# Optimization experiments

Hardware: AMD Instinct MI355X
Metric: run time of the kernel (lower is better)

The kernel has to match this reference:

```python
import jax, jax.numpy as jnp
import numpy as np

DIM = 1024
N_HEADS = 16
N_KV = 4
HEAD_DIM = 64
HIDDEN = 2048
N_EXP = 8
TOP_K = 2
B, T = 2, 1024
EPS = 1e-6


def rmsnorm(x, w):
    rms = jnp.sqrt(jnp.mean(x * x, axis=-1, keepdims=True) + EPS)
    return w * x / rms


def apply_rope(x, cos, sin):
    # x: [B, H, T, D]; cos/sin: [T, D//2]
    Tn = x.shape[2]
    c = cos[None, None, :Tn, :]
    s = sin[None, None, :Tn, :]
    xe = x[..., 0::2]
    xo = x[..., 1::2]
    re = xe * c - xo * s
    ro = xe * s + xo * c
    return jnp.stack([re, ro], axis=-1).reshape(x.shape)


def setup_inputs() -> dict:
    key = jax.random.key(0)
    ks = jax.random.split(key, 12)
    sd = DIM ** -0.5
    x = jax.random.normal(ks[0], (B, T, DIM), dtype=jnp.float32)
    # RoPE tables
    half = HEAD_DIM // 2
    inv_freq = 1.0 / (10000.0 ** (np.arange(0, half, dtype=np.float32) / half))
    pos = np.arange(T, dtype=np.float32)
    ang = np.outer(pos, inv_freq)
    cos = jnp.asarray(np.cos(ang), dtype=jnp.float32)
    sin = jnp.asarray(np.sin(ang), dtype=jnp.float32)
    return {
        "x": x,
        "cos": cos,
        "sin": sin,
        "norm_attn_w": jnp.ones((DIM,), jnp.float32),
        "wq": jax.random.normal(ks[1], (N_HEADS * HEAD_DIM, DIM), jnp.float32) * sd,
        "wk": jax.random.normal(ks[2], (N_KV * HEAD_DIM, DIM), jnp.float32) * sd,
        "wv": jax.random.normal(ks[3], (N_KV * HEAD_DIM, DIM), jnp.float32) * sd,
        "wo": jax.random.normal(ks[4], (DIM, N_HEADS * HEAD_DIM), jnp.float32) * sd,
        "norm_ffn_w": jnp.ones((DIM,), jnp.float32),
        "router_w": jax.random.normal(ks[5], (N_EXP, DIM), jnp.float32) * sd,
        "router_b": jnp.zeros((N_EXP,), jnp.float32),
        "w_gate": jax.random.normal(ks[6], (N_EXP, HIDDEN, DIM), jnp.float32) * sd,
        "w_up": jax.random.normal(ks[7], (N_EXP, HIDDEN, DIM), jnp.float32) * sd,
        "w_down": jax.random.normal(ks[8], (N_EXP, DIM, HIDDEN), jnp.float32) * (HIDDEN ** -0.5),
    }


def attention(x, cos, sin, wq, wk, wv, wo):
    Bn, Tn, _ = x.shape
    q = (x @ wq.T).reshape(Bn, Tn, N_HEADS, HEAD_DIM).transpose(0, 2, 1, 3)
    k = (x @ wk.T).reshape(Bn, Tn, N_KV, HEAD_DIM).transpose(0, 2, 1, 3)
    v = (x @ wv.T).reshape(Bn, Tn, N_KV, HEAD_DIM).transpose(0, 2, 1, 3)
    q = apply_rope(q, cos, sin)
    k = apply_rope(k, cos, sin)
    rep = N_HEADS // N_KV
    k = jnp.repeat(k, rep, axis=1)
    v = jnp.repeat(v, rep, axis=1)
    scale = HEAD_DIM ** -0.5
    scores = jnp.einsum("bhqd,bhkd->bhqk", q, k) * scale
    causal = jnp.triu(jnp.ones((Tn, Tn), dtype=bool), k=1)
    scores = jnp.where(causal[None, None], -jnp.inf, scores)
    attn = jax.nn.softmax(scores, axis=-1)
    out = jnp.einsum("bhqk,bhkd->bhqd", attn, v)
    out = out.transpose(0, 2, 1, 3).reshape(Bn, Tn, N_HEADS * HEAD_DIM)
    return out @ wo.T


def moe(x, router_w, router_b, w_gate, w_up, w_down):
    Bn, Tn, D = x.shape
    flat = x.reshape(-1, D)  # [N, D]
    N = flat.shape[0]
    logits = flat @ router_w.T + router_b
    probs = jax.nn.softmax(logits, axis=-1)
    top_vals, top_idx = jax.lax.top_k(probs, TOP_K)
    top_vals = top_vals / (jnp.sum(top_vals, axis=-1, keepdims=True) + 1e-9)
    # combine weights [N, E]
    comb = jnp.zeros((N, N_EXP), flat.dtype).at[jnp.arange(N)[:, None], top_idx].add(top_vals)
    g = jnp.einsum("nd,ehd->enh", flat, w_gate)
    u = jnp.einsum("nd,ehd->enh", flat, w_up)
    h = jax.nn.silu(g) * u
    eo = jnp.einsum("enh,edh->end", h, w_down)  # [E, N, D]
    out = jnp.einsum("ne,end->nd", comb, eo)
    return out.reshape(Bn, Tn, D)


def reference(x, cos, sin, norm_attn_w, wq, wk, wv, wo, norm_ffn_w, router_w, router_b, w_gate, w_up, w_down):
    x = x + attention(rmsnorm(x, norm_attn_w), cos, sin, wq, wk, wv, wo)
    x = x + moe(rmsnorm(x, norm_ffn_w), router_w, router_b, w_gate, w_up, w_down)
    return x
```

## Files before the change

kernel.cpp:

```cpp
#include <hip/hip_runtime.h>
#include <math.h>

#define N_TOK   2048
#define SEQ     1024
#define DIMM    1024
#define NH      16
#define NKV     4
#define HD      64
#define HID     2048
#define NEXP    8
#define QKVW    1536

typedef __attribute__((ext_vector_type(4))) float f32x4;
typedef __attribute__((ext_vector_type(8))) short s16x8;
typedef unsigned short u16;

__device__ __forceinline__ u16 f2bf(float f) {
    union { float f; unsigned u; } v; v.f = f;
    unsigned r = v.u + 0x7fffu + ((v.u >> 16) & 1u);
    return (u16)(r >> 16);
}
__device__ __forceinline__ float bf2f(u16 h) {
    union { unsigned u; float f; } v; v.u = ((unsigned)h) << 16;
    return v.f;
}

__device__ __forceinline__ f32x4 mfma16(s16x8 a, s16x8 b, f32x4 c) {
    return __builtin_amdgcn_mfma_f32_16x16x32_bf16(a, b, c, 0, 0, 0);
}

__device__ __forceinline__ int lds_byte(int row, int byte_in_row, int swz_key) {
    return row * 128 + (byte_in_row ^ ((swz_key & 7) << 4));
}

__device__ __forceinline__ s16x8 ldfrag(const char* base, int row, int ks, int lane) {
    int b = lds_byte(row, ks * 64 + ((lane >> 4) * 16), row);
    return *(const s16x8*)(base + b);
}

__device__ __forceinline__ void gload16(const void* g, void* l) {
    __builtin_amdgcn_global_load_lds(
        (const __attribute__((address_space(1))) void*)g,
        (__attribute__((address_space(3))) void*)l, 16, 0, 0);
}

__global__ __launch_bounds__(256) void prep1(const float* __restrict__ wq,
    const float* __restrict__ wk, const float* __restrict__ wv, const float* __restrict__ wo,
    u16* __restrict__ hi, u16* __restrict__ lo,
    const float* __restrict__ x, const float* __restrict__ w_na,
    u16* __restrict__ oh, u16* __restrict__ ol)
{
    if (blockIdx.x < 1024) {
        int i = blockIdx.x * 256 + threadIdx.x;
        int stride = 1024 * 256;
        for (; i < 655360; i += stride) {
            const float* in; int j;
            if (i < 262144)      { in = wq; j = i; }
            else if (i < 327680) { in = wk; j = i - 262144; }
            else if (i < 393216) { in = wv; j = i - 327680; }
            else                 { in = wo; j = i - 393216; }
            f32x4 v = __builtin_nontemporal_load((const f32x4*)in + j);
            ushort4 h, l;
            h.x = f2bf(v[0]); h.y = f2bf(v[1]); h.z = f2bf(v[2]); h.w = f2bf(v[3]);
            l.x = f2bf(v[0] - bf2f(h.x)); l.y = f2bf(v[1] - bf2f(h.y));
            l.z = f2bf(v[2] - bf2f(h.z)); l.w = f2bf(v[3] - bf2f(h.w));
            reinterpret_cast<ushort4*>(hi)[i] = h;
            reinterpret_cast<ushort4*>(lo)[i] = l;
        }
    } else {
        int row = blockIdx.x - 1024;
        const float4* xr = reinterpret_cast<const float4*>(x + (size_t)row * DIMM);
        const float4* wr = reinterpret_cast<const float4*>(w_na);
        float4 v = xr[threadIdx.x];
        float ss = v.x*v.x + v.y*v.y + v.z*v.z + v.w*v.w;
#pragma unroll
        for (int off = 32; off; off >>= 1) ss += __shfl_xor(ss, off);
        __shared__ float red[4];
        int wid = threadIdx.x >> 6, lane = threadIdx.x & 63;
        if (lane == 0) red[wid] = ss;
        __syncthreads();
        float tot = red[0] + red[1] + red[2] + red[3];
        float inv = rsqrtf(tot * (1.0f/DIMM) + 1e-6f);
        float4 ww = wr[threadIdx.x];
        float4 o;
        o.x = ww.x * v.x * inv;
        o.y = ww.y * v.y * inv;
        o.z = ww.z * v.z * inv;
        o.w = ww.w * v.w * inv;
        ushort4 h, l;
        h.x = f2bf(o.x); h.y = f2bf(o.y); h.z = f2bf(o.z); h.w = f2bf(o.w);
        l.x = f2bf(o.x - bf2f(h.x)); l.y = f2bf(o.y - bf2f(h.y));
        l.z = f2bf(o.z - bf2f(h.z)); l.w = f2bf(o.w - bf2f(h.w));
        reinterpret_cast<ushort4*>(oh + (size_t)row * DIMM)[threadIdx.x] = h;
        reinterpret_cast<ushort4*>(ol + (size_t)row * DIMM)[threadIdx.x] = l;
    }
}

__global__ __launch_bounds__(256) void rmsnorm_router(const float* __restrict__ x,
    const float* __restrict__ w, const float* __restrict__ rw, const float* __restrict__ rb,
    u16* __restrict__ outb, int* __restrict__ top_idx, float* __restrict__ top_w)
{
    int row = blockIdx.x;
    int tid = threadIdx.x;
    int wid = tid >> 6, lane = tid & 63;
    const float4* xr = reinterpret_cast<const float4*>(x + (size_t)row * DIMM);
    const float4* wr = reinterpret_cast<const float4*>(w);
    float4 v = xr[tid];
    float ss = v.x*v.x + v.y*v.y + v.z*v.z + v.w*v.w;
#pragma unroll
    for (int off = 32; off; off >>= 1) ss += __shfl_xor(ss, off);
    __shared__ float red[4];
    __shared__ float lred[4][NEXP];
    if (lane == 0) red[wid] = ss;
    __syncthreads();
    float tot = red[0] + red[1] + red[2] + red[3];
    float inv = rsqrtf(tot * (1.0f/DIMM) + 1e-6f);
    float4 ww = wr[tid];
    float4 o;
    o.x = ww.x * v.x * inv;
    o.y = ww.y * v.y * inv;
    o.z = ww.z * v.z * inv;
    o.w = ww.w * v.w * inv;
    ushort4 ob;
    ob.x = f2bf(o.x); ob.y = f2bf(o.y); ob.z = f2bf(o.z); ob.w = f2bf(o.w);
    reinterpret_cast<ushort4*>(outb + (size_t)row * DIMM)[tid] = ob;
    float acc[NEXP];
#pragma unroll
    for (int e = 0; e < NEXP; e++) {
        float4 r4 = reinterpret_cast<const float4*>(rw + (size_t)e * DIMM)[tid];
        acc[e] = o.x * r4.x + o.y * r4.y + o.z * r4.z + o.w * r4.w;
    }
#pragma unroll
    for (int e = 0; e < NEXP; e++) {
        float p = acc[e];
#pragma unroll
        for (int off = 32; off; off >>= 1) p += __shfl_xor(p, off);
        acc[e] = p;
    }
    if (lane == 0)
#pragma unroll
        for (int e = 0; e < NEXP; e++) lred[wid][e] = acc[e];
    __syncthreads();
    if (tid == 0) {
        float lg[NEXP];
#pragma unroll
        for (int e = 0; e < NEXP; e++)
            lg[e] = lred[0][e] + lred[1][e] + lred[2][e] + lred[3][e] + rb[e];
        float m = lg[0];
#pragma unroll
        for (int e = 1; e < NEXP; e++) m = fmaxf(m, lg[e]);
        float pe[NEXP], s = 0.f;
#pragma unroll
        for (int e = 0; e < NEXP; e++) { pe[e] = __expf(lg[e] - m); s += pe[e]; }
        int i1 = 0; float v1 = pe[0];
#pragma unroll
        for (int e = 1; e < NEXP; e++) if (pe[e] > v1) { v1 = pe[e]; i1 = e; }
        int i2 = -1; float v2 = -1.f;
#pragma unroll
        for (int e = 0; e < NEXP; e++) if (e != i1 && pe[e] > v2) { v2 = pe[e]; i2 = e; }
        v1 /= s; v2 /= s;
        float den = v1 + v2 + 1e-9f;
        top_idx[2 * row] = i1; top_idx[2 * row + 1] = i2;
        top_w[2 * row] = v1 / den; top_w[2 * row + 1] = v2 / den;
    }
}

__global__ __launch_bounds__(256) void route_build(const int* __restrict__ top_idx,
    const float* __restrict__ top_w, int* __restrict__ counts, int* __restrict__ offs,
    int* __restrict__ assign_token, float* __restrict__ assign_w)
{
    __shared__ int lcnt[NEXP], loff[NEXP], lpos[NEXP];
    int tid = threadIdx.x;
    if (tid < NEXP) { lcnt[tid] = 0; lpos[tid] = 0; }
    __syncthreads();
    for (int i = tid; i < 2 * N_TOK; i += 256)
        atomicAdd(&lcnt[top_idx[i]], 1);
    __syncthreads();
    if (tid == 0) {
        int s = 0;
        for (int e = 0; e < NEXP; e++) { loff[e] = s; s += lcnt[e]; }
    }
    __syncthreads();
    if (tid < NEXP) { counts[tid] = lcnt[tid]; offs[tid] = loff[tid]; }
    for (int i = tid; i < 2 * N_TOK; i += 256) {
        int e = top_idx[i];
        int p = atomicAdd(&lpos[e], 1);
        int r = loff[e] + p;
        assign_token[r] = i >> 1;
        assign_w[r] = top_w[i];
    }
}

__global__ __launch_bounds__(256) void gemm_bs(const u16* __restrict__ Ah_,
    const u16* __restrict__ Al_, const u16* __restrict__ Bh_, const u16* __restrict__ Bl_,
    float* __restrict__ C, const float* __restrict__ R, int M, int N, int K, int ldc)
{
    __shared__ __align__(16) u16 Ah[128 * 64], Al[128 * 64];
    __shared__ __align__(16) u16 Bh[64 * 64],  Bl[64 * 64];
    int tid = threadIdx.x;
    int m0 = blockIdx.y * 128, n0 = blockIdx.x * 64;
    int lane = tid & 63, wv = tid >> 6;
    int wm = wv >> 1, wn = wv & 1;
    int sr = lane >> 3, sc = lane & 7;

    f32x4 acc[4][2];
#pragma unroll
    for (int i = 0; i < 4; i++)
#pragma unroll
        for (int j = 0; j < 2; j++) acc[i][j] = f32x4{0.f, 0.f, 0.f, 0.f};

    const int NT = K >> 6;
    int bid = blockIdx.x + gridDim.x * blockIdx.y;
    int ph = (bid * 5) & (NT - 1);

    for (int tt = 0; tt < NT; ++tt) {
        int k0 = ((tt + ph) & (NT - 1)) << 6;
#pragma unroll
        for (int i = 0; i < 4; i++) {
            int row = wv * 32 + i * 8 + sr;
            int c = sc ^ (row & 7);
            size_t g = (size_t)(m0 + row) * K + k0 + c * 8;
            gload16(Ah_ + g, (void*)(Ah + (wv * 4 + i) * 512));
            gload16(Al_ + g, (void*)(Al + (wv * 4 + i) * 512));
        }
#pragma unroll
        for (int i = 0; i < 2; i++) {
            int row = wv * 16 + i * 8 + sr;
            int c = sc ^ (row & 7);
            size_t g = (size_t)(n0 + row) * K + k0 + c * 8;
            gload16(Bh_ + g, (void*)(Bh + (wv * 2 + i) * 512));
            gload16(Bl_ + g, (void*)(Bl + (wv * 2 + i) * 512));
        }
        __syncthreads();
#pragma unroll
        for (int ks = 0; ks < 2; ++ks) {
            s16x8 afh[4], afl[4], bfh[2], bfl[2];
#pragma unroll
            for (int mi = 0; mi < 4; mi++) {
                int row = wm * 64 + mi * 16 + (lane & 15);
                afh[mi] = ldfrag((const char*)Ah, row, ks, lane);
                afl[mi] = ldfrag((const char*)Al, row, ks, lane);
            }
#pragma unroll
            for (int nj = 0; nj < 2; nj++) {
                int row = wn * 32 + nj * 16 + (lane & 15);
                bfh[nj] = ldfrag((const char*)Bh, row, ks, lane);
                bfl[nj] = ldfrag((const char*)Bl, row, ks, lane);
            }
#pragma unroll
            for (int mi = 0; mi < 4; mi++)
#pragma unroll
                for (int nj = 0; nj < 2; nj++) {
                    acc[mi][nj] = mfma16(afl[mi], bfh[nj], acc[mi][nj]);
                    acc[mi][nj] = mfma16(afh[mi], bfl[nj], acc[mi][nj]);
                    acc[mi][nj] = mfma16(afh[mi], bfh[nj], acc[mi][nj]);
                }
        }
        __syncthreads();
    }
#pragma unroll
    for (int mi = 0; mi < 4; mi++)
#pragma unroll
        for (int nj = 0; nj < 2; nj++)
#pragma unroll
            for (int r = 0; r < 4; r++) {
                int m = m0 + wm * 64 + mi * 16 + (lane >> 4) * 4 + r;
                int n = n0 + wn * 32 + nj * 16 + (lane & 15);
                float v = acc[mi][nj][r];
                if (R) v += R[(size_t)m * ldc + n];
                C[(size_t)m * ldc + n] = v;
            }
}

__global__ __launch_bounds__(256) void prep2(const float* __restrict__ qkvb,
    const float* __restrict__ cs, const float* __restrict__ sn,
    u16* __restrict__ qsh, u16* __restrict__ qsl,
    u16* __restrict__ ksh, u16* __restrict__ ksl,
    u16* __restrict__ vth, u16* __restrict__ vtl)
{
    const int ROPE_BLOCKS = (N_TOK * (NH + NKV) * 32) / 256;
    if (blockIdx.x < ROPE_BLOCKS) {
        int gid = blockIdx.x * 256 + threadIdx.x;
        const int QTOT = N_TOK * NH * 32;
        int nheads, base_col, out_w;
        u16 *oh, *ol;
        if (gid < QTOT) {
            nheads = NH; base_col = 0; out_w = NH * HD; oh = qsh; ol = qsl;
        } else {
            gid -= QTOT;
            nheads = NKV; base_col = 1024; out_w = NKV * HD; oh = ksh; ol = ksl;
        }
        int i = gid & 31;
        int h = (gid >> 5) % nheads;
        int n = gid / (32 * nheads);
        int t = n & (SEQ - 1);
        const float* p = qkvb + (size_t)n * QKVW + base_col + h * HD + 2 * i;
        float xe = p[0], xo = p[1];
        float c = cs[t * 32 + i], s = sn[t * 32 + i];
        float re = xe * c - xo * s;
        float ro = xe * s + xo * c;
        size_t o = (size_t)n * out_w + h * HD + 2 * i;
        u16 reh = f2bf(re), roh = f2bf(ro);
        oh[o] = reh;     oh[o + 1] = roh;
        ol[o] = f2bf(re - bf2f(reh));
        ol[o + 1] = f2bf(ro - bf2f(roh));
    } else {
        __shared__ float t[64][65];
        int r = blockIdx.x - ROPE_BLOCKS;
        int bx = r & 31;
        int by = r >> 5;
        int tid = threadIdx.x;
        int c4 = tid & 15, r0 = tid >> 4;
#pragma unroll
        for (int i = 0; i < 4; i++) {
            int row = r0 + i * 16;
            float4 vv = *(const float4*)(qkvb + (size_t)(bx * 64 + row) * QKVW + 1280 + by * 64 + c4 * 4);
            t[c4 * 4 + 0][row] = vv.x;
            t[c4 * 4 + 1][row] = vv.y;
            t[c4 * 4 + 2][row] = vv.z;
            t[c4 * 4 + 3][row] = vv.w;
        }
        __syncthreads();
#pragma unroll
        for (int i = 0; i < 4; i++) {
            int drow = r0 + i * 16;
            ushort4 hh, ll;
            float a = t[drow][c4 * 4 + 0], b = t[drow][c4 * 4 + 1];
            float c = t[drow][c4 * 4 + 2], d = t[drow][c4 * 4 + 3];
            hh.x = f2bf(a); hh.y = f2bf(b); hh.z = f2bf(c); hh.w = f2bf(d);
            ll.x = f2bf(a - bf2f(hh.x)); ll.y = f2bf(b - bf2f(hh.y));
            ll.z = f2bf(c - bf2f(hh.z)); ll.w = f2bf(d - bf2f(hh.w));
            size_t o = ((size_t)(by * 64 + drow) * N_TOK + bx * 64 + c4 * 4) >> 2;
            reinterpret_cast<ushort4*>(vth)[o] = hh;
            reinterpret_cast<ushort4*>(vtl)[o] = ll;
        }
    }
}

__global__ __launch_bounds__(256) void attn_cvt(const u16* __restrict__ qsh,
    const u16* __restrict__ qsl, const u16* __restrict__ ksh, const u16* __restrict__ ksl,
    const u16* __restrict__ vth, const u16* __restrict__ vtl,
    u16* __restrict__ outh, u16* __restrict__ outl,
    const float* __restrict__ wg, const float* __restrict__ wu, const float* __restrict__ wd,
    u16* __restrict__ wgb, u16* __restrict__ wub, u16* __restrict__ wdb)
{
    if (blockIdx.x >= 512) {
        const int n4 = 4 << 20;
        int i = (blockIdx.x - 512) * 1024 + threadIdx.x;
        int stride = 3072 * 1024;
        for (; i < 3 * n4; i += stride) {
            int seg = i >> 22;
            int j = i & (n4 - 1);
            const f32x4* in = (const f32x4*)((seg == 0) ? wg : (seg == 1) ? wu : wd);
            ushort4* out = (ushort4*)((seg == 0) ? wgb : (seg == 1) ? wub : wdb);
            f32x4 v0 = __builtin_nontemporal_load(in + j);
            f32x4 v1 = __builtin_nontemporal_load(in + j + 256);
            f32x4 v2 = __builtin_nontemporal_load(in + j + 512);
            f32x4 v3 = __builtin_nontemporal_load(in + j + 768);
            ushort4 o0, o1, o2, o3;
            o0.x = f2bf(v0[0]); o0.y = f2bf(v0[1]); o0.z = f2bf(v0[2]); o0.w = f2bf(v0[3]);
            o1.x = f2bf(v1[0]); o1.y = f2bf(v1[1]); o1.z = f2bf(v1[2]); o1.w = f2bf(v1[3]);
            o2.x = f2bf(v2[0]); o2.y = f2bf(v2[1]); o2.z = f2bf(v2[2]); o2.w = f2bf(v2[3]);
            o3.x = f2bf(v3[0]); o3.y = f2bf(v3[1]); o3.z = f2bf(v3[2]); o3.w = f2bf(v3[3]);
            out[j]       = o0;
            out[j + 256] = o1;
            out[j + 512] = o2;
            out[j + 768] = o3;
        }
        return;
    }
    int bi = blockIdx.x;
    int b = bi >> 8;
    int h = (bi >> 4) & 15;
    int qt = 15 - (bi & 15);
    int kvh = h >> 2;
    int tid = threadIdx.x;
    int lane = tid & 63, wv = tid >> 6;
    int q0 = qt * 64;
    int sr = lane >> 3, sc = lane & 7;

    __shared__ __align__(16) u16 Qh[64 * 64], Ql[64 * 64];
    __shared__ __align__(16) u16 Kh[64 * 64], Kl[64 * 64];
    __shared__ __align__(16) u16 Vh[64 * 64], Vl[64 * 64];

#pragma unroll
    for (int i = 0; i < 2; i++) {
        int row = wv * 16 + i * 8 + sr;
        int c = sc ^ (row & 7);
        size_t g = (size_t)(b * SEQ + q0 + row) * (NH * HD) + h * HD + c * 8;
        gload16(qsh + g, (void*)(Qh + (wv * 2 + i) * 512));
        gload16(qsl + g, (void*)(Ql + (wv * 2 + i) * 512));
    }
    __syncthreads();

    s16x8 aQh[2], aQl[2];
#pragma unroll
    for (int ks = 0; ks < 2; ks++) {
        aQh[ks] = ldfrag((const char*)Qh, wv * 16 + (lane & 15), ks, lane);
        aQl[ks] = ldfrag((const char*)Ql, wv * 16 + (lane & 15), ks, lane);
    }

    float m_run[4], l_run[4];
    f32x4 acc_o[4];
#pragma unroll
    for (int r = 0; r < 4; r++) { m_run[r] = -1e30f; l_run[r] = 0.f; }
#pragma unroll
    for (int nj = 0; nj < 4; nj++) acc_o[nj] = f32x4{0.f, 0.f, 0.f, 0.f};

    for (int kt = 0; kt <= qt; kt++) {
        int kbase = kt * 64;
        __syncthreads();
#pragma unroll
        for (int i = 0; i < 2; i++) {
            int row = wv * 16 + i * 8 + sr;
            int c = sc ^ (row & 7);
            size_t gk = (size_t)(b * SEQ + kbase + row) * (NKV * HD) + kvh * HD + c * 8;
            size_t gv = (size_t)(kvh * HD + row) * N_TOK + b * SEQ + kbase + c * 8;
            gload16(ksh + gk, (void*)(Kh + (wv * 2 + i) * 512));
            gload16(ksl + gk, (void*)(Kl + (wv * 2 + i) * 512));
            gload16(vth + gv, (void*)(Vh + (wv * 2 + i) * 512));
            gload16(vtl + gv, (void*)(Vl + (wv * 2 + i) * 512));
        }
        __syncthreads();

        f32x4 sacc[4];
#pragma unroll
        for (int nj = 0; nj < 4; nj++) sacc[nj] = f32x4{0.f, 0.f, 0.f, 0.f};
#pragma unroll
        for (int ks = 0; ks < 2; ks++) {
#pragma unroll
            for (int nj = 0; nj < 4; nj++) {
                s16x8 bKh = ldfrag((const char*)Kh, nj * 16 + (lane & 15), ks, lane);
                s16x8 bKl = ldfrag((const char*)Kl, nj * 16 + (lane & 15), ks, lane);
                sacc[nj] = mfma16(aQl[ks], bKh, sacc[nj]);
                sacc[nj] = mfma16(aQh[ks], bKl, sacc[nj]);
                sacc[nj] = mfma16(aQh[ks], bKh, sacc[nj]);
            }
        }

        float sv[4][4];
#pragma unroll
        for (int nj = 0; nj < 4; nj++)
#pragma unroll
            for (int r = 0; r < 4; r++) {
                float s = sacc[nj][r] * 0.125f;
                if (kt == qt) {
                    int row_loc = wv * 16 + (lane >> 4) * 4 + r;
                    int col_loc = nj * 16 + (lane & 15);
                    if (col_loc > row_loc) s = -1e30f;
                }
                sv[nj][r] = s;
            }

        float p[4][4];
#pragma unroll
        for (int r = 0; r < 4; r++) {
            float mx = fmaxf(fmaxf(sv[0][r], sv[1][r]), fmaxf(sv[2][r], sv[3][r]));
            mx = fmaxf(mx, __shfl_xor(mx, 1));
            mx = fmaxf(mx, __shfl_xor(mx, 2));
            mx = fmaxf(mx, __shfl_xor(mx, 4));
            mx = fmaxf(mx, __shfl_xor(mx, 8));
            float m_new = fmaxf(m_run[r], mx);
            float corr = __expf(m_run[r] - m_new);
            float ps = 0.f;
#pragma unroll
            for (int nj = 0; nj < 4; nj++) {
                float pv = __expf(sv[nj][r] - m_new);
                p[nj][r] = pv;
                ps += pv;
            }
            ps += __shfl_xor(ps, 1);
            ps += __shfl_xor(ps, 2);
            ps += __shfl_xor(ps, 4);
            ps += __shfl_xor(ps, 8);
            l_run[r] = l_run[r] * corr + ps;
            m_run[r] = m_new;
#pragma unroll
            for (int nj = 0; nj < 4; nj++) acc_o[nj][r] *= corr;
        }

        char* phb = (char*)Qh + wv * 2048;
        char* plb = (char*)Ql + wv * 2048;
#pragma unroll
        for (int nj = 0; nj < 4; nj++)
#pragma unroll
            for (int r = 0; r < 4; r++) {
                int row = (lane >> 4) * 4 + r;
                int col = nj * 16 + (lane & 15);
                u16 hh = f2bf(p[nj][r]);
                u16 ll = f2bf(p[nj][r] - bf2f(hh));
                int byte = lds_byte(row, col * 2, row);
                *(u16*)(phb + byte) = hh;
                *(u16*)(plb + byte) = ll;
            }

#pragma unroll
        for (int ks = 0; ks < 2; ks++) {
            s16x8 aPh = ldfrag(phb, lane & 15, ks, lane);
            s16x8 aPl = ldfrag(plb, lane & 15, ks, lane);
#pragma unroll
            for (int nj = 0; nj < 4; nj++) {
                s16x8 bVh = ldfrag((const char*)Vh, nj * 16 + (lane & 15), ks, lane);
                s16x8 bVl = ldfrag((const char*)Vl, nj * 16 + (lane & 15), ks, lane);
                acc_o[nj] = mfma16(aPl, bVh, acc_o[nj]);
                acc_o[nj] = mfma16(aPh, bVl, acc_o[nj]);
                acc_o[nj] = mfma16(aPh, bVh, acc_o[nj]);
            }
        }
    }

#pragma unroll
    for (int r = 0; r < 4; r++) {
        int row_glob = q0 + wv * 16 + (lane >> 4) * 4 + r;
        float inv = 1.f / l_run[r];
#pragma unroll
        for (int nj = 0; nj < 4; nj++) {
            int dv = nj * 16 + (lane & 15);
            size_t idx = (size_t)(b * SEQ + row_glob) * (NH * HD) + h * HD + dv;
            float v = acc_o[nj][r] * inv;
            u16 hh = f2bf(v);
            outh[idx] = hh;
            outl[idx] = f2bf(v - bf2f(hh));
        }
    }
}

__global__ __launch_bounds__(256) void moe_gateup2(const u16* __restrict__ xb,
    const u16* __restrict__ wgb, const u16* __restrict__ wub,
    const int* __restrict__ assign_token, const int* __restrict__ offs,
    const int* __restrict__ counts, u16* __restrict__ hbufb)
{
    int e = blockIdx.z;
    int cnt = counts[e];
    int t0 = blockIdx.y * 128;
    if (t0 >= cnt) return;
    int base = offs[e];
    int h0 = blockIdx.x * 64;
    __shared__ __align__(16) u16 As[128 * 64];
    __shared__ __align__(16) u16 Gs[64 * 64];
    __shared__ __align__(16) u16 Us[64 * 64];
    __shared__ int toks[128];
    int tid = threadIdx.x;
    if (tid < 128) {
        int a = t0 + tid;
        toks[tid] = (a < cnt) ? assign_token[base + a] : 0;
    }
    __syncthreads();
    int lane = tid & 63, wv = tid >> 6;
    int wm = wv >> 1, wn = wv & 1;
    int sr = lane >> 3, sc = lane & 7;

    int tokr[4];
#pragma unroll
    for (int i = 0; i < 4; i++) tokr[i] = toks[wv * 32 + i * 8 + sr];

    const u16* wge = wgb + (size_t)e * HID * DIMM;
    const u16* wue = wub + (size_t)e * HID * DIMM;

    f32x4 accg[4][2], accu[4][2];
#pragma unroll
    for (int i = 0; i < 4; i++)
#pragma unroll
        for (int j = 0; j < 2; j++) { accg[i][j] = f32x4{0,0,0,0}; accu[i][j] = f32x4{0,0,0,0}; }

    const int NT = DIMM / 64;
    int bid = blockIdx.x + gridDim.x * (blockIdx.y + gridDim.y * blockIdx.z);
    int ph = (bid * 5) & (NT - 1);

    for (int tt = 0; tt < NT; ++tt) {
        int k0 = ((tt + ph) & (NT - 1)) << 6;
#pragma unroll
        for (int i = 0; i < 4; i++) {
            int row = wv * 32 + i * 8 + sr;
            int c = sc ^ (row & 7);
            gload16(xb + (size_t)tokr[i] * DIMM + k0 + c * 8, (void*)(As + (wv * 4 + i) * 512));
        }
#pragma unroll
        for (int i = 0; i < 2; i++) {
            int row = wv * 16 + i * 8 + sr;
            int c = sc ^ (row & 7);
            gload16(wge + (size_t)(h0 + row) * DIMM + k0 + c * 8, (void*)(Gs + (wv * 2 + i) * 512));
            gload16(wue + (size_t)(h0 + row) * DIMM + k0 + c * 8, (void*)(Us + (wv * 2 + i) * 512));
        }
        __syncthreads();
#pragma unroll
        for (int ks = 0; ks < 2; ++ks) {
            s16x8 af[4], gf[2], uf[2];
#pragma unroll
            for (int mi = 0; mi < 4; mi++)
                af[mi] = ldfrag((const char*)As, wm * 64 + mi * 16 + (lane & 15), ks, lane);
#pragma unroll
            for (int nj = 0; nj < 2; nj++) {
                int row = wn * 32 + nj * 16 + (lane & 15);
                gf[nj] = ldfrag((const char*)Gs, row, ks, lane);
                uf[nj] = ldfrag((const char*)Us, row, ks, lane);
            }
#pragma unroll
            for (int mi = 0; mi < 4; mi++)
#pragma unroll
                for (int nj = 0; nj < 2; nj++) {
                    accg[mi][nj] = mfma16(af[mi], gf[nj], accg[mi][nj]);
                    accu[mi][nj] = mfma16(af[mi], uf[nj], accu[mi][nj]);
                }
        }
        __syncthreads();
    }
#pragma unroll
    for (int mi = 0; mi < 4; mi++)
#pragma unroll
        for (int nj = 0; nj < 2; nj++)
#pragma unroll
            for (int r = 0; r < 4; r++) {
                int row = wm * 64 + mi * 16 + (lane >> 4) * 4 + r;
                if (t0 + row < cnt) {
                    int col = wn * 32 + nj * 16 + (lane & 15);
                    float g = accg[mi][nj][r], u = accu[mi][nj][r];
                    float hh = (g / (1.f + __expf(-g))) * u;
                    hbufb[(size_t)(base + t0 + row) * HID + h0 + col] = f2bf(hh);
                }
            }
}

__global__ __launch_bounds__(256) void moe_down2(const u16* __restrict__ hbufb,
    const u16* __restrict__ wdb, const int* __restrict__ assign_token,
    const float* __restrict__ assign_w, const int* __restrict__ offs,
    const int* __restrict__ counts, float* __restrict__ out)
{
    int e = blockIdx.z;
    int cnt = counts[e];
    int t0 = blockIdx.y * 128;
    if (t0 >= cnt) return;
    int base = offs[e];
    int d0 = blockIdx.x * 128;
    __shared__ __align__(16) u16 As[128 * 64];
    __shared__ __align__(16) u16 Bs[128 * 64];
    __shared__ int toks[128];
    __shared__ float rw_[128];
    int tid = threadIdx.x;
    if (tid < 128) {
        int a = t0 + tid;
        toks[tid] = (a < cnt) ? assign_token[base + a] : 0;
        rw_[tid] = (a < cnt) ? assign_w[base + a] : 0.f;
    }
    __syncthreads();
    int lane = tid & 63, wv = tid >> 6;
    int wm = wv >> 1, wn = wv & 1;
    int sr = lane >> 3, sc = lane & 7;

    const u16* wde = wdb + (size_t)e * DIMM * HID;

    f32x4 acc[4][4];
#pragma unroll
    for (int i = 0; i < 4; i++)
#pragma unroll
        for (int j = 0; j < 4; j++) acc[i][j] = f32x4{0,0,0,0};

    const int NT = HID / 64;
    int bid = blockIdx.x + gridDim.x * (blockIdx.y + gridDim.y * blockIdx.z);
    int ph = (bid * 5) & (NT - 1);

    for (int tt = 0; tt < NT; ++tt) {
        int k0 = ((tt + ph) & (NT - 1)) << 6;
#pragma unroll
        for (int i = 0; i < 4; i++) {
            int row = wv * 32 + i * 8 + sr;
            int c = sc ^ (row & 7);
            gload16(hbufb + (size_t)(base + t0 + row) * HID + k0 + c * 8, (void*)(As + (wv * 4 + i) * 512));
            gload16(wde + (size_t)(d0 + row) * HID + k0 + c * 8, (void*)(Bs + (wv * 4 + i) * 512));
        }
        __syncthreads();
#pragma unroll
        for (int ks = 0; ks < 2; ++ks) {
            s16x8 af[4];
#pragma unroll
            for (int mi = 0; mi < 4; mi++)
                af[mi] = ldfrag((const char*)As, wm * 64 + mi * 16 + (lane & 15), ks, lane);
#pragma unroll
            for (int nj = 0; nj < 4; nj++) {
                s16x8 bf = ldfrag((const char*)Bs, wn * 64 + nj * 16 + (lane & 15), ks, lane);
#pragma unroll
                for (int mi = 0; mi < 4; mi++)
                    acc[mi][nj] = mfma16(af[mi], bf, acc[mi][nj]);
            }
        }
        __syncthreads();
    }
#pragma unroll
    for (int mi = 0; mi < 4; mi++)
#pragma unroll
        for (int r = 0; r < 4; r++) {
            int row = wm * 64 + mi * 16 + (lane >> 4) * 4 + r;
            if (t0 + row < cnt) {
                int tok = toks[row];
                float w = rw_[row];
#pragma unroll
                for (int nj = 0; nj < 4; nj++) {
                    int col = d0 + wn * 64 + nj * 16 + (lane & 15);
                    atomicAdd(&out[(size_t)tok * DIMM + col], acc[mi][nj][r] * w);
                }
            }
        }
}

extern "C" void kernel_launch(void* const* d_in, const int* in_sizes, int n_in,
                              void* d_out, int out_size, void* d_ws, size_t ws_size,
                              hipStream_t stream)
{
    const float* x      = (const float*)d_in[0];
    const float* cs     = (const float*)d_in[1];
    const float* sn     = (const float*)d_in[2];
    const float* w_na   = (const float*)d_in[3];
    const float* wq     = (const float*)d_in[4];
    const float* wk     = (const float*)d_in[5];
    const float* wv     = (const float*)d_in[6];
    const float* wo     = (const float*)d_in[7];
    const float* w_nf   = (const float*)d_in[8];
    const float* rw     = (const float*)d_in[9];
    const float* rb     = (const float*)d_in[10];
    const float* wg     = (const float*)d_in[11];
    const float* wu     = (const float*)d_in[12];
    const float* wd     = (const float*)d_in[13];
    float* out = (float*)d_out;

    const size_t F = 1024 * 1024;
    float* wsf = (float*)d_ws;

    float* qkvb = wsf;
    float* tail = wsf + 3 * F;
    u16* qsh    = (u16*)(wsf + 3 * F + F / 2);
    u16* qsl    = (u16*)(wsf + 4 * F + F / 2);
    u16* ksh    = (u16*)(wsf + 5 * F + F / 2);
    u16* ksl    = (u16*)(wsf + 5 * F + 3 * F / 4);
    u16* vth    = (u16*)(wsf + 6 * F);
    u16* vtl    = (u16*)(wsf + 6 * F + F / 4);
    u16* xn2b   = (u16*)(wsf + 6 * F + F / 2);
    u16* hbufb  = (u16*)(wsf + 7 * F + F / 2);
    u16* xnh    = (u16*)(wsf + 7 * F + F / 2);
    u16* xnl    = (u16*)(wsf + 8 * F + F / 2);
    u16* attnh  = (u16*)(wsf + 9 * F + F / 2);
    u16* attnl  = (u16*)(wsf + 10 * F + F / 2);
    u16* wgb    = (u16*)(wsf + 11 * F + F / 2);
    u16* wub    = (u16*)(wsf + 19 * F + F / 2);
    u16* wdb    = (u16*)(wsf + 27 * F + F / 2);
    u16* wqkvoh = (u16*)(wsf + 35 * F + F / 2);
    u16* wqkvol = (u16*)(wsf + 36 * F + 3 * F / 4);

    int*   top_idx      = (int*)tail;
    float* top_w        = tail + 4096;
    int*   counts       = (int*)(tail + 8192);
    int*   offs         = (int*)(tail + 8192) + 8;
    int*   assign_token = (int*)(tail + 8192) + 32;
    float* assign_w     = tail + 8192 + 32 + 4096;

    prep1<<<3072, 256, 0, stream>>>(wq, wk, wv, wo, wqkvoh, wqkvol, x, w_na, xnh, xnl);
    gemm_bs<<<dim3(QKVW / 64, 16), 256, 0, stream>>>(xnh, xnl, wqkvoh, wqkvol,
                                                     qkvb, nullptr, N_TOK, QKVW, DIMM, QKVW);
    prep2<<<5248, 256, 0, stream>>>(qkvb, cs, sn, qsh, qsl, ksh, ksl, vth, vtl);
    attn_cvt<<<3584, 256, 0, stream>>>(qsh, qsl, ksh, ksl, vth, vtl, attnh, attnl,
                                       wg, wu, wd, wgb, wub, wdb);
    gemm_bs<<<dim3(DIMM / 64, 16), 256, 0, stream>>>(attnh, attnl,
                                                     wqkvoh + (size_t)1536 * 1024, wqkvol + (size_t)1536 * 1024,
                                                     out, x, N_TOK, DIMM, NH * HD, DIMM);
    rmsnorm_router<<<N_TOK, 256, 0, stream>>>(out, w_nf, rw, rb, xn2b, top_idx, top_w);
    route_build<<<1, 256, 0, stream>>>(top_idx, top_w, counts, offs, assign_token, assign_w);
    moe_gateup2<<<dim3(HID / 64, 16, NEXP), 256, 0, stream>>>(xn2b, wgb, wub, assign_token, offs, counts, hbufb);
    moe_down2<<<dim3(DIMM / 128, 16, NEXP), 256, 0, stream>>>(hbufb, wdb, assign_token, assign_w, offs, counts, out);
}
```

Baseline: 314.5 us.

## Spread MoE weight bf16 conversion across QKV gemm, attention and out-proj kernels

The fp32-to-bf16 conversion of the expert weights used to run only as extra blocks inside the attention kernel. It is now split into three ranges, handled by extra blocks appended to the QKV projection GEMM, the attention kernel and the output projection GEMM. The GEMM grid is flattened to 1D so conversion blocks can share the launch. The aim is to hide the memory-bound conversion behind the compute-bound kernels. The risk is that conversion traffic slows the GEMMs, and the extra blocks change how blocks are scheduled.

Result: faster. 302.2 us, median of 2 (-3.9%).

```diff
diff --git a/kernel.cpp b/kernel.cpp
--- a/kernel.cpp
+++ b/kernel.cpp
@@ -42,6 +42,34 @@
     __builtin_amdgcn_global_load_lds(
         (const __attribute__((address_space(1))) void*)g,
         (__attribute__((address_space(3))) void*)l, 16, 0, 0);
+}
+
+__device__ __forceinline__ void cvt_chunk(int cb, int ncvt, int cvt_base, int cvt_end,
+    const float* __restrict__ wg, const float* __restrict__ wu, const float* __restrict__ wd,
+    u16* __restrict__ wgb, u16* __restrict__ wub, u16* __restrict__ wdb, int tid)
+{
+    const int n4 = 4 << 20;
+    int i = cvt_base + cb * 1024 + tid;
+    int stride = ncvt * 1024;
+    for (; i < cvt_end; i += stride) {
+        int seg = i >> 22;
+        int j = i & (n4 - 1);
+        const f32x4* in = (const f32x4*)((seg == 0) ? wg : (seg == 1) ? wu : wd);
+        ushort4* out = (ushort4*)((seg == 0) ? wgb : (seg == 1) ? wub : wdb);
+        f32x4 v0 = __builtin_nontemporal_load(in + j);
+        f32x4 v1 = __builtin_nontemporal_load(in + j + 256);
+        f32x4 v2 = __builtin_nontemporal_load(in + j + 512);
+        f32x4 v3 = __builtin_nontemporal_load(in + j + 768);
+        ushort4 o0, o1, o2, o3;
+        o0.x = f2bf(v0[0]); o0.y = f2bf(v0[1]); o0.z = f2bf(v0[2]); o0.w = f2bf(v0[3]);
+        o1.x = f2bf(v1[0]); o1.y = f2bf(v1[1]); o1.z = f2bf(v1[2]); o1.w = f2bf(v1[3]);
+        o2.x = f2bf(v2[0]); o2.y = f2bf(v2[1]); o2.z = f2bf(v2[2]); o2.w = f2bf(v2[3]);
+        o3.x = f2bf(v3[0]); o3.y = f2bf(v3[1]); o3.z = f2bf(v3[2]); o3.w = f2bf(v3[3]);
+        out[j]       = o0;
+        out[j + 256] = o1;
+        out[j + 512] = o2;
+        out[j + 768] = o3;
+    }
 }
 
 __global__ __launch_bounds__(256) void prep1(const float* __restrict__ wq,
@@ -191,14 +219,23 @@
     }
 }
 
-__global__ __launch_bounds__(256) void gemm_bs(const u16* __restrict__ Ah_,
+__global__ __launch_bounds__(256) void gemm_cvt(const u16* __restrict__ Ah_,
     const u16* __restrict__ Al_, const u16* __restrict__ Bh_, const u16* __restrict__ Bl_,
-    float* __restrict__ C, const float* __restrict__ R, int M, int N, int K, int ldc)
-{
+    float* __restrict__ C, const float* __restrict__ R, int M, int N, int K, int ldc,
+    int gx, int gy,
+    const float* __restrict__ wg, const float* __restrict__ wu, const float* __restrict__ wd,
+    u16* __restrict__ wgb, u16* __restrict__ wub, u16* __restrict__ wdb,
+    int cvt_base, int cvt_end, int ncvt)
+{
+    int blk = blockIdx.x;
+    if (blk >= gx * gy) {
+        cvt_chunk(blk - gx * gy, ncvt, cvt_base, cvt_end, wg, wu, wd, wgb, wub, wdb, threadIdx.x);
+        return;
+    }
     __shared__ __align__(16) u16 Ah[128 * 64], Al[128 * 64];
     __shared__ __align__(16) u16 Bh[64 * 64],  Bl[64 * 64];
     int tid = threadIdx.x;
-    int m0 = blockIdx.y * 128, n0 = blockIdx.x * 64;
+    int m0 = (blk / gx) * 128, n0 = (blk % gx) * 64;
     int lane = tid & 63, wv = tid >> 6;
     int wm = wv >> 1, wn = wv & 1;
     int sr = lane >> 3, sc = lane & 7;
@@ -210,8 +247,7 @@
         for (int j = 0; j < 2; j++) acc[i][j] = f32x4{0.f, 0.f, 0.f, 0.f};
 
     const int NT = K >> 6;
-    int bid = blockIdx.x + gridDim.x * blockIdx.y;
-    int ph = (bid * 5) & (NT - 1);
+    int ph = (blk * 5) & (NT - 1);
 
     for (int tt = 0; tt < NT; ++tt) {
         int k0 = ((tt + ph) & (NT - 1)) << 6;
@@ -342,31 +378,11 @@
     const u16* __restrict__ vth, const u16* __restrict__ vtl,
     u16* __restrict__ outh, u16* __restrict__ outl,
     const float* __restrict__ wg, const float* __restrict__ wu, const float* __restrict__ wd,
-    u16* __restrict__ wgb, u16* __restrict__ wub, u16* __restrict__ wdb)
+    u16* __restrict__ wgb, u16* __restrict__ wub, u16* __restrict__ wdb,
+    int cvt_base, int cvt_end, int ncvt)
 {
     if (blockIdx.x >= 512) {
-        const int n4 = 4 << 20;
-        int i = (blockIdx.x - 512) * 1024 + threadIdx.x;
-        int stride = 3072 * 1024;
-        for (; i < 3 * n4; i += stride) {
-            int seg = i >> 22;
-            int j = i & (n4 - 1);
-            const f32x4* in = (const f32x4*)((seg == 0) ? wg : (seg == 1) ? wu : wd);
-            ushort4* out = (ushort4*)((seg == 0) ? wgb : (seg == 1) ? wub : wdb);
-            f32x4 v0 = __builtin_nontemporal_load(in + j);
-            f32x4 v1 = __builtin_nontemporal_load(in + j + 256);
-            f32x4 v2 = __builtin_nontemporal_load(in + j + 512);
-            f32x4 v3 = __builtin_nontemporal_load(in + j + 768);
-            ushort4 o0, o1, o2, o3;
-            o0.x = f2bf(v0[0]); o0.y = f2bf(v0[1]); o0.z = f2bf(v0[2]); o0.w = f2bf(v0[3]);
-            o1.x = f2bf(v1[0]); o1.y = f2bf(v1[1]); o1.z = f2bf(v1[2]); o1.w = f2bf(v1[3]);
-            o2.x = f2bf(v2[0]); o2.y = f2bf(v2[1]); o2.z = f2bf(v2[2]); o2.w = f2bf(v2[3]);
-            o3.x = f2bf(v3[0]); o3.y = f2bf(v3[1]); o3.z = f2bf(v3[2]); o3.w = f2bf(v3[3]);
-            out[j]       = o0;
-            out[j + 256] = o1;
-            out[j + 512] = o2;
-            out[j + 768] = o3;
-        }
+        cvt_chunk(blockIdx.x - 512, ncvt, cvt_base, cvt_end, wg, wu, wd, wgb, wub, wdb, threadIdx.x);
         return;
     }
     int bi = blockIdx.x;
@@ -752,15 +768,23 @@
     int*   assign_token = (int*)(tail + 8192) + 32;
     float* assign_w     = tail + 8192 + 32 + 4096;
 
+    const int CV1 = 5242880;
+    const int CV2 = 9437184;
+    const int CV3 = 12582912;
+
     prep1<<<3072, 256, 0, stream>>>(wq, wk, wv, wo, wqkvoh, wqkvol, x, w_na, xnh, xnl);
-    gemm_bs<<<dim3(QKVW / 64, 16), 256, 0, stream>>>(xnh, xnl, wqkvoh, wqkvol,
-                                                     qkvb, nullptr, N_TOK, QKVW, DIMM, QKVW);
+    gemm_cvt<<<384 + 1280, 256, 0, stream>>>(xnh, xnl, wqkvoh, wqkvol,
+                                             qkvb, nullptr, N_TOK, QKVW, DIMM, QKVW,
+                                             QKVW / 64, 16,
+                                             wg, wu, wd, wgb, wub, wdb, 0, CV1, 1280);
     prep2<<<5248, 256, 0, stream>>>(qkvb, cs, sn, qsh, qsl, ksh, ksl, vth, vtl);
-    attn_cvt<<<3584, 256, 0, stream>>>(qsh, qsl, ksh, ksl, vth, vtl, attnh, attnl,
-                                       wg, wu, wd, wgb, wub, wdb);
-    gemm_bs<<<dim3(DIMM / 64, 16), 256, 0, stream>>>(attnh, attnl,
-                                                     wqkvoh + (size_t)1536 * 1024, wqkvol + (size_t)1536 * 1024,
-                                                     out, x, N_TOK, DIMM, NH * HD, DIMM);
+    attn_cvt<<<1536, 256, 0, stream>>>(qsh, qsl, ksh, ksl, vth, vtl, attnh, attnl,
+                                       wg, wu, wd, wgb, wub, wdb, CV1, CV2, 1024);
+    gemm_cvt<<<256 + 768, 256, 0, stream>>>(attnh, attnl,
+                                            wqkvoh + (size_t)1536 * 1024, wqkvol + (size_t)1536 * 1024,
+                                            out, x, N_TOK, DIMM, NH * HD, DIMM,
+                                            DIMM / 64, 16,
+                                            wg, wu, wd, wgb, wub, wdb, CV2, CV3, 768);
     rmsnorm_router<<<N_TOK, 256, 0, stream>>>(out, w_nf, rw, rb, xn2b, top_idx, top_w);
     route_build<<<1, 256, 0, stream>>>(top_idx, top_w, counts, offs, assign_token, assign_w);
     moe_gateup2<<<dim3(HID / 64, 16, NEXP), 256, 0, stream>>>(xn2b, wgb, wub, assign_token, offs, counts, hbufb);
```
